# Kernel tuning notes

Hardware: AMD Instinct MI355X
Metric: run time of the kernel (lower is better)

The kernel has to match this reference:

```python
import jax, jax.numpy as jnp
import numpy as np

CROP = (7, 7)
CANONICAL = 56.0
MIN_LEVEL, MAX_LEVEL = 0, 4


def _crop_and_resize(feat, boxes, box_idx, ch, cw):
    # feat: [B,H,W,C]; boxes: [N,4] interpreted as (y1,x1,y2,x2) in [0,1]
    # TF tf.image.crop_and_resize bilinear semantics, extrapolation_value=0
    B, H, W, C = feat.shape
    y1, x1, y2, x2 = boxes[:, 0], boxes[:, 1], boxes[:, 2], boxes[:, 3]
    Hf, Wf = float(H - 1), float(W - 1)
    gy = jnp.arange(ch, dtype=boxes.dtype)
    gx = jnp.arange(cw, dtype=boxes.dtype)
    ys = y1[:, None] * Hf + gy[None, :] * ((y2 - y1) * Hf / (ch - 1))[:, None]  # [N,ch]
    xs = x1[:, None] * Wf + gx[None, :] * ((x2 - x1) * Wf / (cw - 1))[:, None]  # [N,cw]
    y0f = jnp.floor(ys)
    x0f = jnp.floor(xs)
    ly = (ys - y0f)[:, :, None, None]  # [N,ch,1,1]
    lx = (xs - x0f)[:, None, :, None]  # [N,1,cw,1]
    y0 = jnp.clip(y0f, 0.0, Hf).astype(jnp.int32)
    y1i = jnp.clip(y0f + 1.0, 0.0, Hf).astype(jnp.int32)
    x0 = jnp.clip(x0f, 0.0, Wf).astype(jnp.int32)
    x1i = jnp.clip(x0f + 1.0, 0.0, Wf).astype(jnp.int32)
    b = box_idx[:, None, None]
    v00 = feat[b, y0[:, :, None], x0[:, None, :]]   # [N,ch,cw,C]
    v01 = feat[b, y0[:, :, None], x1i[:, None, :]]
    v10 = feat[b, y1i[:, :, None], x0[:, None, :]]
    v11 = feat[b, y1i[:, :, None], x1i[:, None, :]]
    top = v00 + lx * (v01 - v00)
    bot = v10 + lx * (v11 - v10)
    val = top + ly * (bot - top)
    ok = ((ys >= 0) & (ys <= Hf))[:, :, None] & ((xs >= 0) & (xs <= Wf))[:, None, :]
    return jnp.where(ok[..., None], val, jnp.zeros((), val.dtype))


def _roi_align(boxes, feats, image_shape):
    B, N, _ = boxes.shape
    # source: x1,y1,x2,y2 = split(boxes); h = y2-y1; w = x2-x1
    h = boxes[..., 3] - boxes[..., 1]
    w = boxes[..., 2] - boxes[..., 0]
    area = (image_shape[0] * image_shape[1]).astype(jnp.float32)
    lvl = jnp.log2(jnp.sqrt(h * w) / (CANONICAL / jnp.sqrt(area)))
    lvl = jnp.clip(jnp.round(lvl).astype(jnp.int32), MIN_LEVEL, MAX_LEVEL)  # [B,N]
    # source passes raw boxes to crop_and_resize (interpreted as y1,x1,y2,x2)
    bf = jax.lax.stop_gradient(boxes.reshape(B * N, 4))
    bidx = jnp.repeat(jnp.arange(B, dtype=jnp.int32), N)
    # crops from every level for every box, then select the assigned level
    crops = jnp.stack([_crop_and_resize(f, bf, bidx, CROP[0], CROP[1]) for f in feats])  # [L,BN,7,7,C]
    sel = (lvl.reshape(B * N) - MIN_LEVEL)[None, :, None, None, None]
    pooled = jnp.take_along_axis(crops, sel, axis=0)[0]  # [BN,7,7,C]
    return pooled.reshape(B, N, CROP[0], CROP[1], feats[0].shape[-1])


def setup_inputs() -> dict:
    key = jax.random.key(0)
    kx, ky, kw, kh, k0, k1, k2, k3, k4 = jax.random.split(key, 9)
    B, N, C = 2, 1000, 256
    cx = jax.random.uniform(kx, (B, N), minval=0.25, maxval=0.75)
    cy = jax.random.uniform(ky, (B, N), minval=0.25, maxval=0.75)
    bw = jax.random.uniform(kw, (B, N), minval=0.02, maxval=0.5)
    bh = jax.random.uniform(kh, (B, N), minval=0.02, maxval=0.5)
    x1 = cx - bw / 2.0
    x2 = cx + bw / 2.0
    y1 = cy - bh / 2.0
    y2 = cy + bh / 2.0
    boxes = jnp.stack([x1, y1, x2, y2], axis=-1).astype(jnp.float32)  # [B,N,4]
    sizes = [256, 128, 64, 32, 16]
    feats = [jax.random.normal(k, (B, s, s, C), dtype=jnp.float32)
             for k, s in zip([k0, k1, k2, k3, k4], sizes)]
    return {
        "boxes": boxes,
        "feat0": feats[0], "feat1": feats[1], "feat2": feats[2],
        "feat3": feats[3], "feat4": feats[4],
        "image_shape": jnp.array([1024, 1024], dtype=jnp.int32),
    }


def reference(boxes, feat0, feat1, feat2, feat3, feat4, image_shape):
    return _roi_align(boxes, [feat0, feat1, feat2, feat3, feat4], image_shape)
```

## Files before the change

### kernel.cpp

```cpp
#include <hip/hip_runtime.h>
#include <math.h>

#define CCH 256
#define CROP 7

__global__ __launch_bounds__(64) void roi_align_kernel(
    const float4* __restrict__ boxes,
    const float* __restrict__ f0,
    const float* __restrict__ f1,
    const float* __restrict__ f2,
    const float* __restrict__ f3,
    const float* __restrict__ f4,
    const int*  __restrict__ image_shape,
    float* __restrict__ out,
    int N)
{
    const int cell = blockIdx.x;
    const int bn   = blockIdx.y;
    const int c4   = threadIdx.x;
    const int iy   = cell / CROP;
    const int ix   = cell % CROP;
    const int b    = bn / N;

    const float4 box = boxes[bn];
    const float ry1 = box.x;
    const float cx1 = box.y;
    const float ry2 = box.z;
    const float cx2 = box.w;

    const float h = cx2 - cx1;
    const float w = ry2 - ry1;

    const float area  = (float)(image_shape[0] * image_shape[1]);
    const float canon = 56.0f / sqrtf(area);
    const float lvlf  = log2f(sqrtf(h * w) / canon);
    int lvl = (int)rintf(lvlf);
    lvl = lvl < 0 ? 0 : (lvl > 4 ? 4 : lvl);

    const float* f; int s;
    if      (lvl == 0) { f = f0; s = 256; }
    else if (lvl == 1) { f = f1; s = 128; }
    else if (lvl == 2) { f = f2; s = 64;  }
    else if (lvl == 3) { f = f3; s = 32;  }
    else               { f = f4; s = 16;  }

    const float Hf = (float)(s - 1);
    const float Wf = Hf;

    const float ystep = (ry2 - ry1) * Hf / 6.0f;
    const float xstep = (cx2 - cx1) * Wf / 6.0f;
    const float ys = ry1 * Hf + (float)iy * ystep;
    const float xs = cx1 * Wf + (float)ix * xstep;

    const float y0f = floorf(ys);
    const float x0f = floorf(xs);
    const float ly = ys - y0f;
    const float lx = xs - x0f;

    const int y0  = (int)fminf(fmaxf(y0f,        0.0f), Hf);
    const int y1i = (int)fminf(fmaxf(y0f + 1.0f, 0.0f), Hf);
    const int x0  = (int)fminf(fmaxf(x0f,        0.0f), Wf);
    const int x1i = (int)fminf(fmaxf(x0f + 1.0f, 0.0f), Wf);

    const bool ok = (ys >= 0.0f) && (ys <= Hf) && (xs >= 0.0f) && (xs <= Wf);

    const size_t img  = (size_t)b * s * s * CCH;
    const size_t o00  = img + ((size_t)y0  * s + x0 ) * CCH;
    const size_t o01  = img + ((size_t)y0  * s + x1i) * CCH;
    const size_t o10  = img + ((size_t)y1i * s + x0 ) * CCH;
    const size_t o11  = img + ((size_t)y1i * s + x1i) * CCH;

    const float4 v00 = *((const float4*)(f + o00) + c4);
    const float4 v01 = *((const float4*)(f + o01) + c4);
    const float4 v10 = *((const float4*)(f + o10) + c4);
    const float4 v11 = *((const float4*)(f + o11) + c4);

    float4 val;
    {
        float tx = v00.x + lx * (v01.x - v00.x);
        float bx = v10.x + lx * (v11.x - v10.x);
        val.x = tx + ly * (bx - tx);
        float ty = v00.y + lx * (v01.y - v00.y);
        float by = v10.y + lx * (v11.y - v10.y);
        val.y = ty + ly * (by - ty);
        float tz = v00.z + lx * (v01.z - v00.z);
        float bz = v10.z + lx * (v11.z - v10.z);
        val.z = tz + ly * (bz - tz);
        float tw = v00.w + lx * (v01.w - v00.w);
        float bw = v10.w + lx * (v11.w - v10.w);
        val.w = tw + ly * (bw - tw);
    }
    if (!ok) { val.x = 0.0f; val.y = 0.0f; val.z = 0.0f; val.w = 0.0f; }

    float4* optr = (float4*)(out + ((size_t)bn * (CROP * CROP) + cell) * CCH) + c4;
    *optr = val;
}

extern "C" void kernel_launch(void* const* d_in, const int* in_sizes, int n_in,
                              void* d_out, int out_size, void* d_ws, size_t ws_size,
                              hipStream_t stream) {
    const float4* boxes = (const float4*)d_in[0];
    const float*  f0    = (const float*)d_in[1];
    const float*  f1    = (const float*)d_in[2];
    const float*  f2    = (const float*)d_in[3];
    const float*  f3    = (const float*)d_in[4];
    const float*  f4    = (const float*)d_in[5];
    const int*    ishp  = (const int*)d_in[6];
    float*        out   = (float*)d_out;

    const int BN = in_sizes[0] / 4;
    const int B  = in_sizes[1] / (256 * 256 * 256);
    const int N  = BN / B;

    dim3 grid(CROP * CROP, BN);
    roi_align_kernel<<<grid, 64, 0, stream>>>(boxes, f0, f1, f2, f3, f4, ishp, out, N);
}
```

Before: 248.9 us.

## Process one box per block with four waves, two cells per iteration

Restructures the grid from one 64-thread block per (cell, box) to one 256-thread block per box. Each wave handles pairs of crop cells, issuing eight float4 gathers before interpolating so more loads are in flight. Output goes through nontemporal stores. This amortizes the per-box level computation and launch overhead across all 49 cells, at the cost of fewer blocks and a slightly uneven split of cells across waves.

```diff
diff --git a/kernel.cpp b/kernel.cpp
--- a/kernel.cpp
+++ b/kernel.cpp
@@ -3,9 +3,51 @@
 
 #define CCH 256
 #define CROP 7
+#define NCELL 49
 
-__global__ __launch_bounds__(64) void roi_align_kernel(
-    const float4* __restrict__ boxes,
+typedef float f32x4 __attribute__((ext_vector_type(4)));
+
+#define CELL_ADDR(S, cell)                                                        \
+    const int   iy##S  = (cell) / CROP;                                           \
+    const int   ix##S  = (cell) % CROP;                                           \
+    const float ys##S  = ry1 * Hf + (float)iy##S * ystep;                         \
+    const float xs##S  = cx1 * Hf + (float)ix##S * xstep;                         \
+    const float y0f##S = floorf(ys##S);                                           \
+    const float x0f##S = floorf(xs##S);                                           \
+    const float ly##S  = ys##S - y0f##S;                                          \
+    const float lx##S  = xs##S - x0f##S;                                          \
+    const int   y0##S  = (int)fminf(fmaxf(y0f##S,        0.0f), Hf);              \
+    const int   y1i##S = (int)fminf(fmaxf(y0f##S + 1.0f, 0.0f), Hf);              \
+    const int   x0##S  = (int)fminf(fmaxf(x0f##S,        0.0f), Hf);              \
+    const int   x1i##S = (int)fminf(fmaxf(x0f##S + 1.0f, 0.0f), Hf);              \
+    const bool  ok##S  = (ys##S >= 0.0f) && (ys##S <= Hf) &&                      \
+                         (xs##S >= 0.0f) && (xs##S <= Hf);                        \
+    const f32x4* p00##S = (const f32x4*)(f + img + ((size_t)y0##S  * s + x0##S ) * CCH) + c4; \
+    const f32x4* p01##S = (const f32x4*)(f + img + ((size_t)y0##S  * s + x1i##S) * CCH) + c4; \
+    const f32x4* p10##S = (const f32x4*)(f + img + ((size_t)y1i##S * s + x0##S ) * CCH) + c4; \
+    const f32x4* p11##S = (const f32x4*)(f + img + ((size_t)y1i##S * s + x1i##S) * CCH) + c4;
+
+#define LERP_STORE(S, v00, v01, v10, v11, cell)                                   \
+    {                                                                             \
+        f32x4 val;                                                                \
+        float tx = v00.x + lx##S * (v01.x - v00.x);                               \
+        float bx = v10.x + lx##S * (v11.x - v10.x);                               \
+        val.x = tx + ly##S * (bx - tx);                                           \
+        float ty = v00.y + lx##S * (v01.y - v00.y);                               \
+        float by = v10.y + lx##S * (v11.y - v10.y);                               \
+        val.y = ty + ly##S * (by - ty);                                           \
+        float tz = v00.z + lx##S * (v01.z - v00.z);                               \
+        float bz = v10.z + lx##S * (v11.z - v10.z);                               \
+        val.z = tz + ly##S * (bz - tz);                                           \
+        float tw = v00.w + lx##S * (v01.w - v00.w);                               \
+        float bw = v10.w + lx##S * (v11.w - v10.w);                               \
+        val.w = tw + ly##S * (bw - tw);                                           \
+        if (!ok##S) { val.x = 0.0f; val.y = 0.0f; val.z = 0.0f; val.w = 0.0f; }   \
+        __builtin_nontemporal_store(val, outbn + (size_t)(cell) * (CCH / 4));     \
+    }
+
+__global__ __launch_bounds__(256, 4) void roi_align_kernel(
+    const f32x4* __restrict__ boxes,
     const float* __restrict__ f0,
     const float* __restrict__ f1,
     const float* __restrict__ f2,
@@ -15,14 +57,12 @@
     float* __restrict__ out,
     int N)
 {
-    const int cell = blockIdx.x;
-    const int bn   = blockIdx.y;
-    const int c4   = threadIdx.x;
-    const int iy   = cell / CROP;
-    const int ix   = cell % CROP;
+    const int bn   = blockIdx.x;
+    const int wave = threadIdx.x >> 6;
+    const int c4   = threadIdx.x & 63;
     const int b    = bn / N;
 
-    const float4 box = boxes[bn];
+    const f32x4 box = boxes[bn];
     const float ry1 = box.x;
     const float cx1 = box.y;
     const float ry2 = box.z;
@@ -45,61 +85,36 @@
     else               { f = f4; s = 16;  }
 
     const float Hf = (float)(s - 1);
-    const float Wf = Hf;
+    const float ystep = (ry2 - ry1) * Hf / 6.0f;
+    const float xstep = (cx2 - cx1) * Hf / 6.0f;
 
-    const float ystep = (ry2 - ry1) * Hf / 6.0f;
-    const float xstep = (cx2 - cx1) * Wf / 6.0f;
-    const float ys = ry1 * Hf + (float)iy * ystep;
-    const float xs = cx1 * Wf + (float)ix * xstep;
+    const size_t img = (size_t)b * s * s * CCH;
+    f32x4* outbn = (f32x4*)(out + (size_t)bn * (NCELL * CCH)) + c4;
 
-    const float y0f = floorf(ys);
-    const float x0f = floorf(xs);
-    const float ly = ys - y0f;
-    const float lx = xs - x0f;
+    for (int base = wave * 2; base < NCELL; base += 8) {
+        const int  cA   = base;
+        const bool hasB = (base + 1) < NCELL;
+        const int  cB   = hasB ? base + 1 : base;
 
-    const int y0  = (int)fminf(fmaxf(y0f,        0.0f), Hf);
-    const int y1i = (int)fminf(fmaxf(y0f + 1.0f, 0.0f), Hf);
-    const int x0  = (int)fminf(fmaxf(x0f,        0.0f), Wf);
-    const int x1i = (int)fminf(fmaxf(x0f + 1.0f, 0.0f), Wf);
+        CELL_ADDR(A, cA)
+        CELL_ADDR(B, cB)
 
-    const bool ok = (ys >= 0.0f) && (ys <= Hf) && (xs >= 0.0f) && (xs <= Wf);
+        const f32x4 a00 = *p00A; const f32x4 a01 = *p01A;
+        const f32x4 a10 = *p10A; const f32x4 a11 = *p11A;
+        const f32x4 b00 = *p00B; const f32x4 b01 = *p01B;
+        const f32x4 b10 = *p10B; const f32x4 b11 = *p11B;
 
-    const size_t img  = (size_t)b * s * s * CCH;
-    const size_t o00  = img + ((size_t)y0  * s + x0 ) * CCH;
-    const size_t o01  = img + ((size_t)y0  * s + x1i) * CCH;
-    const size_t o10  = img + ((size_t)y1i * s + x0 ) * CCH;
-    const size_t o11  = img + ((size_t)y1i * s + x1i) * CCH;
-
-    const float4 v00 = *((const float4*)(f + o00) + c4);
-    const float4 v01 = *((const float4*)(f + o01) + c4);
-    const float4 v10 = *((const float4*)(f + o10) + c4);
-    const float4 v11 = *((const float4*)(f + o11) + c4);
-
-    float4 val;
-    {
-        float tx = v00.x + lx * (v01.x - v00.x);
-        float bx = v10.x + lx * (v11.x - v10.x);
-        val.x = tx + ly * (bx - tx);
-        float ty = v00.y + lx * (v01.y - v00.y);
-        float by = v10.y + lx * (v11.y - v10.y);
-        val.y = ty + ly * (by - ty);
-        float tz = v00.z + lx * (v01.z - v00.z);
-        float bz = v10.z + lx * (v11.z - v10.z);
-        val.z = tz + ly * (bz - tz);
-        float tw = v00.w + lx * (v01.w - v00.w);
-        float bw = v10.w + lx * (v11.w - v10.w);
-        val.w = tw + ly * (bw - tw);
+        LERP_STORE(A, a00, a01, a10, a11, cA)
+        if (hasB) {
+            LERP_STORE(B, b00, b01, b10, b11, cB)
+        }
     }
-    if (!ok) { val.x = 0.0f; val.y = 0.0f; val.z = 0.0f; val.w = 0.0f; }
-
-    float4* optr = (float4*)(out + ((size_t)bn * (CROP * CROP) + cell) * CCH) + c4;
-    *optr = val;
 }
 
 extern "C" void kernel_launch(void* const* d_in, const int* in_sizes, int n_in,
                               void* d_out, int out_size, void* d_ws, size_t ws_size,
                               hipStream_t stream) {
-    const float4* boxes = (const float4*)d_in[0];
+    const f32x4*  boxes = (const f32x4*)d_in[0];
     const float*  f0    = (const float*)d_in[1];
     const float*  f1    = (const float*)d_in[2];
     const float*  f2    = (const float*)d_in[3];
@@ -112,6 +127,6 @@
     const int B  = in_sizes[1] / (256 * 256 * 256);
     const int N  = BN / B;
 
-    dim3 grid(CROP * CROP, BN);
-    roi_align_kernel<<<grid, 64, 0, stream>>>(boxes, f0, f1, f2, f3, f4, ishp, out, N);
+    dim3 grid(BN);
+    roi_align_kernel<<<grid, 256, 0, stream>>>(boxes, f0, f1, f2, f3, f4, ishp, out, N);
 }
```

Measured after the change: 263.2 us. 1.06x slower.
